# Kernel tuning notes

Measured on AMD Instinct MI355X. Metric: run time of the kernel, lower is better.

## Reference

```python
import jax, jax.numpy as jnp
import numpy as np

EPS = 1e-12  # tf.math.l2_normalize default epsilon

def l2norm(x, axis=-1):
    s = jnp.sum(x * x, axis=axis, keepdims=True)
    return x * jax.lax.rsqrt(jnp.maximum(s, EPS))

def setup_inputs() -> dict:
    key = jax.random.key(0)
    ks = jax.random.split(key, 8)
    B, N, M, D_IN, D_OUT = 8, 4096, 2048, 256, 128
    Y = jax.random.normal(ks[0], (B, N, D_IN), dtype=jnp.float32)
    indices_ = jax.random.randint(ks[1], (B, M), 0, N)
    he = lambda k, fan_in, shape: jax.random.normal(k, shape, jnp.float32) * jnp.sqrt(2.0 / fan_in)
    kernel_query = he(ks[2], D_IN, (D_IN, D_OUT))
    b_query = jnp.zeros((D_OUT,), jnp.float32)
    kernel_key = he(ks[3], D_IN, (D_IN, D_OUT))
    b_key = jnp.zeros((D_OUT,), jnp.float32)
    kernel_value_w = he(ks[4], D_IN, (D_IN, D_OUT))
    kernel_value_b = jnp.zeros((D_OUT,), jnp.float32)
    return {"Y": Y, "indices_": indices_, "kernel_query": kernel_query, "b_query": b_query,
            "kernel_key": kernel_key, "b_key": b_key,
            "kernel_value_w": kernel_value_w, "kernel_value_b": kernel_value_b}

def reference(Y, indices_, kernel_query, b_query, kernel_key, b_key, kernel_value_w, kernel_value_b):
    # Gather same indices for Q/K/V (queries=keys=values=Y in the self block)
    g = jnp.take_along_axis(Y, indices_[..., None], axis=1)      # [B, m, d_in]
    d_in = Y.shape[-1]                                           # scale uses pre-projection dim (as in source)
    Q = jnp.einsum('bmd,de->bme', g, kernel_query) + b_query     # [B, m, d_out]
    K = jnp.einsum('bmd,de->bme', g, kernel_key) + b_key
    V = jax.nn.relu(jnp.einsum('bmd,de->bme', g, kernel_value_w) + kernel_value_b)
    scores = jnp.einsum('bme,bne->bmn', Q, K) / jnp.sqrt(jnp.float32(d_in))  # [B, m, m]
    att = jax.nn.softmax(scores, axis=-1)                        # valid_lens=None path -> plain softmax
    att_emb = l2norm(jnp.einsum('bmn,bne->bme', att, V))         # attention_embedding: l2-normalize, not sum-divide
    out = l2norm(V + att_emb)                                    # residual_connection with l2 normalize
    return (out, att)
```

## Files before the change

### kernel.cpp

```cpp
#include <hip/hip_runtime.h>
#include <hip/hip_bf16.h>
#include <math.h>

typedef __attribute__((ext_vector_type(8))) short short8;
typedef __attribute__((ext_vector_type(16))) float f32x16;

constexpr int B = 8, N = 4096, M = 2048, DIN = 256, DOUT = 128;
constexpr float SCORE_SCALE = 0.0625f;

__device__ __forceinline__ unsigned short f2b(float x) {
    unsigned int u = __builtin_bit_cast(unsigned int, x);
    u += 0x7fffu + ((u >> 16) & 1u);
    return (unsigned short)(u >> 16);
}

__global__ __launch_bounds__(128) void k_proj(
    const float* __restrict__ Y, const int* __restrict__ idx,
    const float* __restrict__ Wq, const float* __restrict__ bq,
    const float* __restrict__ Wk, const float* __restrict__ bk,
    const float* __restrict__ Wv, const float* __restrict__ bv,
    unsigned short* __restrict__ Qb, unsigned short* __restrict__ Kb,
    unsigned short* __restrict__ Vb, float* __restrict__ Vf)
{
    constexpr int TM = 8;
    __shared__ float g[TM][DIN];
    const int rm0 = blockIdx.x * TM;
    const int b = rm0 / M;
    const int t = threadIdx.x;
    #pragma unroll
    for (int r = 0; r < TM; ++r) {
        const int id = idx[rm0 + r];
        const float2* src = (const float2*)(Y + ((size_t)b * N + id) * DIN);
        ((float2*)g[r])[t] = src[t];
    }
    __syncthreads();

    float aq[TM], ak[TM], av[TM];
    #pragma unroll
    for (int r = 0; r < TM; ++r) { aq[r] = 0.f; ak[r] = 0.f; av[r] = 0.f; }

    for (int d = 0; d < DIN; d += 4) {
        float wq[4], wk[4], wv[4];
        #pragma unroll
        for (int u = 0; u < 4; ++u) {
            wq[u] = Wq[(d + u) * DOUT + t];
            wk[u] = Wk[(d + u) * DOUT + t];
            wv[u] = Wv[(d + u) * DOUT + t];
        }
        #pragma unroll
        for (int r = 0; r < TM; ++r) {
            const float4 gv = *(const float4*)&g[r][d];
            aq[r] = fmaf(gv.x, wq[0], fmaf(gv.y, wq[1], fmaf(gv.z, wq[2], fmaf(gv.w, wq[3], aq[r]))));
            ak[r] = fmaf(gv.x, wk[0], fmaf(gv.y, wk[1], fmaf(gv.z, wk[2], fmaf(gv.w, wk[3], ak[r]))));
            av[r] = fmaf(gv.x, wv[0], fmaf(gv.y, wv[1], fmaf(gv.z, wv[2], fmaf(gv.w, wv[3], av[r]))));
        }
    }
    #pragma unroll
    for (int r = 0; r < TM; ++r) {
        const size_t o = (size_t)(rm0 + r) * DOUT + t;
        const float q = aq[r] + bq[t];
        const float k = ak[r] + bk[t];
        const float v = fmaxf(av[r] + bv[t], 0.0f);
        Qb[o] = f2b(q);
        Kb[o] = f2b(k);
        Vb[o] = f2b(v);
        Vf[o] = v;
    }
}

#define SMEM_BYTES 99328

__global__ __launch_bounds__(512) void k_attn(
    const unsigned short* __restrict__ Qb, const unsigned short* __restrict__ Kb,
    const unsigned short* __restrict__ Vb, const float* __restrict__ Vf,
    float* __restrict__ out, float* __restrict__ att)
{
    extern __shared__ char smem[];
    char* Qs = smem;
    char* Ks = smem + 16384;
    char* Ps = smem + 49152;
    char* Vt = smem + 65536;
    float* sums = (float*)(smem + 98304);

    const int t = threadIdx.x;
    const int l = t & 63, wv = t >> 6;
    const int h = l >> 5;
    const int b = blockIdx.y;
    const int m0 = blockIdx.x * 64;
    const size_t bM = (size_t)b * M;

    const int mw = wv >> 2, nw = wv & 3;
    const int amw = wv & 1, aew = wv >> 1;

    int rowf[16];
    #pragma unroll
    for (int r = 0; r < 16; ++r) rowf[r] = (r & 3) + 8 * (r >> 2) + 4 * h;

    {
        const int row = t >> 3, ce = (t & 7) * 16;
        const uint4* src = (const uint4*)(Qb + (bM + m0 + row) * 128 + ce);
        const uint4 q0 = src[0], q1 = src[1];
        *(uint4*)(Qs + row * 256 + ((ce * 2)      ^ ((row & 7) << 4))) = q0;
        *(uint4*)(Qs + row * 256 + ((ce * 2 + 16) ^ ((row & 7) << 4))) = q1;
    }

    const int krow = t >> 2, kce = (t & 3) * 32;
    const int vrow = t & 127, veb = (t >> 7) * 32;
    const int arow = mw * 32 + (l & 31);
    const int brow = nw * 32 + (l & 31);
    const int kb0 = h * 16;

    uint4 kreg[4], vreg[4];
    {
        const uint4* src = (const uint4*)(Kb + (bM + krow) * 128 + kce);
        #pragma unroll
        for (int u = 0; u < 4; ++u) kreg[u] = src[u];
    }

    float sum_part[16];
    #pragma unroll
    for (int r = 0; r < 16; ++r) sum_part[r] = 0.f;

    for (int c = 0; c < 16; ++c) {
        __syncthreads();
        #pragma unroll
        for (int u = 0; u < 4; ++u)
            *(uint4*)(Ks + krow * 256 + ((kce * 2 + u * 16) ^ ((krow & 7) << 4))) = kreg[u];
        __syncthreads();
        if (c < 15) {
            const uint4* src = (const uint4*)(Kb + (bM + (c + 1) * 128 + krow) * 128 + kce);
            #pragma unroll
            for (int u = 0; u < 4; ++u) kreg[u] = src[u];
        }
        f32x16 acc;
        #pragma unroll
        for (int i = 0; i < 16; ++i) acc[i] = 0.f;
        #pragma unroll
        for (int kc = 0; kc < 8; ++kc) {
            const short8 a  = *(const short8*)(Qs + arow * 256 + ((kc * 32 + kb0) ^ ((arow & 7) << 4)));
            const short8 bb = *(const short8*)(Ks + brow * 256 + ((kc * 32 + kb0) ^ ((brow & 7) << 4)));
            acc = __builtin_amdgcn_mfma_f32_32x32x16_bf16(a, bb, acc, 0, 0, 0);
        }
        #pragma unroll
        for (int r = 0; r < 16; ++r)
            sum_part[r] += __expf(acc[r] * SCORE_SCALE);
    }

    #pragma unroll
    for (int r = 0; r < 16; ++r) {
        float s = sum_part[r];
        #pragma unroll
        for (int off = 1; off <= 16; off <<= 1) s += __shfl_xor(s, off, 64);
        sum_part[r] = s;
    }
    if ((l & 31) == 0) {
        #pragma unroll
        for (int r = 0; r < 16; ++r) sums[nw * 64 + mw * 32 + rowf[r]] = sum_part[r];
    }
    __syncthreads();
    float inv_s[16];
    #pragma unroll
    for (int r = 0; r < 16; ++r) {
        const int rw = mw * 32 + rowf[r];
        inv_s[r] = 1.0f / (sums[rw] + sums[64 + rw] + sums[128 + rw] + sums[192 + rw]);
    }

    {
        const uint4* sk = (const uint4*)(Kb + (bM + krow) * 128 + kce);
        #pragma unroll
        for (int u = 0; u < 4; ++u) kreg[u] = sk[u];
        const uint4* sv = (const uint4*)(Vb + (bM + vrow) * 128 + veb);
        #pragma unroll
        for (int u = 0; u < 4; ++u) vreg[u] = sv[u];
    }
    f32x16 accv;
    #pragma unroll
    for (int i = 0; i < 16; ++i) accv[i] = 0.f;

    float* attb = att + bM * M;
    const int parow = amw * 32 + (l & 31);
    const int vbrow = aew * 32 + (l & 31);

    for (int c = 0; c < 16; ++c) {
        __syncthreads();
        #pragma unroll
        for (int u = 0; u < 4; ++u)
            *(uint4*)(Ks + krow * 256 + ((kce * 2 + u * 16) ^ ((krow & 7) << 4))) = kreg[u];
        #pragma unroll
        for (int u = 0; u < 4; ++u) {
            union { uint4 q; unsigned short us[8]; } cv; cv.q = vreg[u];
            #pragma unroll
            for (int j = 0; j < 8; ++j) {
                const int e = veb + u * 8 + j;
                *(unsigned short*)(Vt + e * 256 + ((vrow * 2) ^ ((e & 7) << 4))) = cv.us[j];
            }
        }
        __syncthreads();
        if (c < 15) {
            const uint4* sk = (const uint4*)(Kb + (bM + (c + 1) * 128 + krow) * 128 + kce);
            #pragma unroll
            for (int u = 0; u < 4; ++u) kreg[u] = sk[u];
            const uint4* sv = (const uint4*)(Vb + (bM + (c + 1) * 128 + vrow) * 128 + veb);
            #pragma unroll
            for (int u = 0; u < 4; ++u) vreg[u] = sv[u];
        }
        f32x16 acc;
        #pragma unroll
        for (int i = 0; i < 16; ++i) acc[i] = 0.f;
        #pragma unroll
        for (int kc = 0; kc < 8; ++kc) {
            const short8 a  = *(const short8*)(Qs + arow * 256 + ((kc * 32 + kb0) ^ ((arow & 7) << 4)));
            const short8 bb = *(const short8*)(Ks + brow * 256 + ((kc * 32 + kb0) ^ ((brow & 7) << 4)));
            acc = __builtin_amdgcn_mfma_f32_32x32x16_bf16(a, bb, acc, 0, 0, 0);
        }
        const int ncol = c * 128 + nw * 32 + (l & 31);
        #pragma unroll
        for (int r = 0; r < 16; ++r) {
            const float p = __expf(acc[r] * SCORE_SCALE) * inv_s[r];
            const int prow = mw * 32 + rowf[r];
            attb[(size_t)(m0 + prow) * M + ncol] = p;
            *(unsigned short*)(Ps + prow * 256 + (((nw * 32 + (l & 31)) * 2) ^ ((prow & 7) << 4))) = f2b(p);
        }
        __syncthreads();
        #pragma unroll
        for (int kc = 0; kc < 8; ++kc) {
            const short8 pa = *(const short8*)(Ps + parow * 256 + ((kc * 32 + kb0) ^ ((parow & 7) << 4)));
            const short8 vb = *(const short8*)(Vt + vbrow * 256 + ((kc * 32 + kb0) ^ ((vbrow & 7) << 4)));
            accv = __builtin_amdgcn_mfma_f32_32x32x16_bf16(pa, vb, accv, 0, 0, 0);
        }
    }

    __syncthreads();
    float* Es = (float*)smem;
    #pragma unroll
    for (int r = 0; r < 16; ++r)
        Es[(amw * 32 + rowf[r]) * 129 + aew * 32 + (l & 31)] = accv[r];
    __syncthreads();
    #pragma unroll
    for (int rr = 0; rr < 8; ++rr) {
        const int row = wv * 8 + rr;
        const float e0 = Es[row * 129 + l];
        const float e1 = Es[row * 129 + l + 64];
        float ss = fmaf(e0, e0, e1 * e1);
        #pragma unroll
        for (int off = 32; off >= 1; off >>= 1) ss += __shfl_xor(ss, off, 64);
        const float rs = rsqrtf(fmaxf(ss, 1e-12f));
        const float v0 = Vf[(bM + m0 + row) * 128 + l];
        const float v1 = Vf[(bM + m0 + row) * 128 + l + 64];
        const float t0 = v0 + e0 * rs, t1 = v1 + e1 * rs;
        float s2 = fmaf(t0, t0, t1 * t1);
        #pragma unroll
        for (int off = 32; off >= 1; off >>= 1) s2 += __shfl_xor(s2, off, 64);
        const float rs2 = rsqrtf(fmaxf(s2, 1e-12f));
        const size_t o = (bM + m0 + row) * 128;
        out[o + l] = t0 * rs2;
        out[o + l + 64] = t1 * rs2;
    }
}

extern "C" void kernel_launch(void* const* d_in, const int* in_sizes, int n_in,
                              void* d_out, int out_size, void* d_ws, size_t ws_size,
                              hipStream_t stream)
{
    const float* Y  = (const float*)d_in[0];
    const int*  idx = (const int*)d_in[1];
    const float* Wq = (const float*)d_in[2];
    const float* bq = (const float*)d_in[3];
    const float* Wk = (const float*)d_in[4];
    const float* bk = (const float*)d_in[5];
    const float* Wv = (const float*)d_in[6];
    const float* bv = (const float*)d_in[7];

    float* out = (float*)d_out;
    float* att = out + (size_t)B * M * DOUT;

    unsigned short* Qb = (unsigned short*)d_ws;
    unsigned short* Kb = Qb + (size_t)B * M * DOUT;
    unsigned short* Vb = Kb + (size_t)B * M * DOUT;
    float*          Vf = (float*)(Vb + (size_t)B * M * DOUT);

    hipFuncSetAttribute((const void*)k_attn, hipFuncAttributeMaxDynamicSharedMemorySize, SMEM_BYTES);

    k_proj<<<B * M / 8, 128, 0, stream>>>(Y, idx, Wq, bq, Wk, bk, Wv, bv, Qb, Kb, Vb, Vf);
    k_attn<<<dim3(M / 64, B), 512, SMEM_BYTES, stream>>>(Qb, Kb, Vb, Vf, out, att);
}
```

Before: 325.4 us.

## Load Q/K/V MFMA fragments directly from global and pre-transpose V in projection

Result: faster. 307.1 us (-5.6%).

```diff
diff --git a/kernel.cpp b/kernel.cpp
--- a/kernel.cpp
+++ b/kernel.cpp
@@ -14,136 +14,132 @@
     return (unsigned short)(u >> 16);
 }
 
-__global__ __launch_bounds__(128) void k_proj(
+__global__ __launch_bounds__(512) void k_proj(
     const float* __restrict__ Y, const int* __restrict__ idx,
     const float* __restrict__ Wq, const float* __restrict__ bq,
     const float* __restrict__ Wk, const float* __restrict__ bk,
     const float* __restrict__ Wv, const float* __restrict__ bv,
     unsigned short* __restrict__ Qb, unsigned short* __restrict__ Kb,
-    unsigned short* __restrict__ Vb, float* __restrict__ Vf)
+    unsigned short* __restrict__ Vbt, float* __restrict__ Vf)
 {
-    constexpr int TM = 8;
-    __shared__ float g[TM][DIN];
-    const int rm0 = blockIdx.x * TM;
-    const int b = rm0 / M;
+    __shared__ float g[32][DIN];
+    const int b = blockIdx.x;
+    const int m0 = blockIdx.y * 32;
     const int t = threadIdx.x;
-    #pragma unroll
-    for (int r = 0; r < TM; ++r) {
-        const int id = idx[rm0 + r];
-        const float2* src = (const float2*)(Y + ((size_t)b * N + id) * DIN);
-        ((float2*)g[r])[t] = src[t];
+    const int e = t & 127, q = t >> 7;
+
+    {
+        const int gr = t >> 4, gc = t & 15;
+        const int id = idx[b * M + m0 + gr];
+        const float4* src = (const float4*)(Y + ((size_t)b * N + id) * DIN);
+        float4* dst = (float4*)g[gr];
+        #pragma unroll
+        for (int j = 0; j < 4; ++j) dst[gc + 16 * j] = src[gc + 16 * j];
     }
     __syncthreads();
 
-    float aq[TM], ak[TM], av[TM];
-    #pragma unroll
-    for (int r = 0; r < TM; ++r) { aq[r] = 0.f; ak[r] = 0.f; av[r] = 0.f; }
+    float aq[8], ak[8], av[8];
+    #pragma unroll
+    for (int r = 0; r < 8; ++r) { aq[r] = 0.f; ak[r] = 0.f; av[r] = 0.f; }
 
     for (int d = 0; d < DIN; d += 4) {
         float wq[4], wk[4], wv[4];
         #pragma unroll
         for (int u = 0; u < 4; ++u) {
-            wq[u] = Wq[(d + u) * DOUT + t];
-            wk[u] = Wk[(d + u) * DOUT + t];
-            wv[u] = Wv[(d + u) * DOUT + t];
-        }
-        #pragma unroll
-        for (int r = 0; r < TM; ++r) {
-            const float4 gv = *(const float4*)&g[r][d];
+            wq[u] = Wq[(d + u) * DOUT + e];
+            wk[u] = Wk[(d + u) * DOUT + e];
+            wv[u] = Wv[(d + u) * DOUT + e];
+        }
+        #pragma unroll
+        for (int r = 0; r < 8; ++r) {
+            const float4 gv = *(const float4*)&g[q * 8 + r][d];
             aq[r] = fmaf(gv.x, wq[0], fmaf(gv.y, wq[1], fmaf(gv.z, wq[2], fmaf(gv.w, wq[3], aq[r]))));
             ak[r] = fmaf(gv.x, wk[0], fmaf(gv.y, wk[1], fmaf(gv.z, wk[2], fmaf(gv.w, wk[3], ak[r]))));
             av[r] = fmaf(gv.x, wv[0], fmaf(gv.y, wv[1], fmaf(gv.z, wv[2], fmaf(gv.w, wv[3], av[r]))));
         }
     }
-    #pragma unroll
-    for (int r = 0; r < TM; ++r) {
-        const size_t o = (size_t)(rm0 + r) * DOUT + t;
-        const float q = aq[r] + bq[t];
-        const float k = ak[r] + bk[t];
-        const float v = fmaxf(av[r] + bv[t], 0.0f);
-        Qb[o] = f2b(q);
-        Kb[o] = f2b(k);
-        Vb[o] = f2b(v);
-        Vf[o] = v;
-    }
-}
-
-#define SMEM_BYTES 99328
-
-__global__ __launch_bounds__(512) void k_attn(
+
+    const float bqe = bq[e], bke = bk[e], bve = bv[e];
+    unsigned short vus[8];
+    #pragma unroll
+    for (int r = 0; r < 8; ++r) {
+        const size_t o = ((size_t)b * M + m0 + q * 8 + r) * DOUT + e;
+        const float qv = aq[r] + bqe;
+        const float kv = ak[r] + bke;
+        const float vv = fmaxf(av[r] + bve, 0.0f);
+        Qb[o] = f2b(qv);
+        Kb[o] = f2b(kv);
+        Vf[o] = vv;
+        vus[r] = f2b(vv);
+    }
+    *(uint4*)(Vbt + ((size_t)b * DOUT + e) * M + m0 + q * 8) = *(uint4*)vus;
+}
+
+__global__ __launch_bounds__(256) void k_attn(
     const unsigned short* __restrict__ Qb, const unsigned short* __restrict__ Kb,
-    const unsigned short* __restrict__ Vb, const float* __restrict__ Vf,
+    const unsigned short* __restrict__ Vbt, const float* __restrict__ Vf,
     float* __restrict__ out, float* __restrict__ att)
 {
-    extern __shared__ char smem[];
-    char* Qs = smem;
-    char* Ks = smem + 16384;
-    char* Ps = smem + 49152;
-    char* Vt = smem + 65536;
-    float* sums = (float*)(smem + 98304);
+    __shared__ char Ps[32 * 256];
+    __shared__ float Es[32][132];
+    __shared__ float sums[4][32];
 
     const int t = threadIdx.x;
     const int l = t & 63, wv = t >> 6;
-    const int h = l >> 5;
-    const int b = blockIdx.y;
-    const int m0 = blockIdx.x * 64;
+    const int h = l >> 5, ln = l & 31;
+    const int b = blockIdx.x;
+    const int m0 = blockIdx.y * 32;
     const size_t bM = (size_t)b * M;
-
-    const int mw = wv >> 2, nw = wv & 3;
-    const int amw = wv & 1, aew = wv >> 1;
+    const int nw = wv;
+    const int ew = wv;
 
     int rowf[16];
     #pragma unroll
     for (int r = 0; r < 16; ++r) rowf[r] = (r & 3) + 8 * (r >> 2) + 4 * h;
 
+    short8 qf[8];
     {
-        const int row = t >> 3, ce = (t & 7) * 16;
-        const uint4* src = (const uint4*)(Qb + (bM + m0 + row) * 128 + ce);
-        const uint4 q0 = src[0], q1 = src[1];
-        *(uint4*)(Qs + row * 256 + ((ce * 2)      ^ ((row & 7) << 4))) = q0;
-        *(uint4*)(Qs + row * 256 + ((ce * 2 + 16) ^ ((row & 7) << 4))) = q1;
-    }
-
-    const int krow = t >> 2, kce = (t & 3) * 32;
-    const int vrow = t & 127, veb = (t >> 7) * 32;
-    const int arow = mw * 32 + (l & 31);
-    const int brow = nw * 32 + (l & 31);
-    const int kb0 = h * 16;
-
-    uint4 kreg[4], vreg[4];
-    {
-        const uint4* src = (const uint4*)(Kb + (bM + krow) * 128 + kce);
-        #pragma unroll
-        for (int u = 0; u < 4; ++u) kreg[u] = src[u];
-    }
-
+        const unsigned short* qrow = Qb + (bM + m0 + ln) * DOUT + h * 8;
+        #pragma unroll
+        for (int kc = 0; kc < 8; ++kc) qf[kc] = *(const short8*)(qrow + kc * 16);
+    }
+
+    const unsigned short* Kbase = Kb + (bM + nw * 32 + ln) * DOUT + h * 8;
+    const unsigned short* Vbase = Vbt + ((size_t)b * DOUT + ew * 32 + ln) * M + h * 8;
+
+    short8 kf0[8], kf1[8];
+    #pragma unroll
+    for (int kc = 0; kc < 8; ++kc) kf0[kc] = *(const short8*)(Kbase + kc * 16);
     float sum_part[16];
     #pragma unroll
     for (int r = 0; r < 16; ++r) sum_part[r] = 0.f;
 
-    for (int c = 0; c < 16; ++c) {
-        __syncthreads();
-        #pragma unroll
-        for (int u = 0; u < 4; ++u)
-            *(uint4*)(Ks + krow * 256 + ((kce * 2 + u * 16) ^ ((krow & 7) << 4))) = kreg[u];
-        __syncthreads();
-        if (c < 15) {
-            const uint4* src = (const uint4*)(Kb + (bM + (c + 1) * 128 + krow) * 128 + kce);
+    #pragma unroll 1
+    for (int cp = 0; cp < 8; ++cp) {
+        const int c0 = cp * 2;
+        #pragma unroll
+        for (int kc = 0; kc < 8; ++kc)
+            kf1[kc] = *(const short8*)(Kbase + (size_t)(c0 + 1) * 128 * DOUT + kc * 16);
+        f32x16 acc;
+        #pragma unroll
+        for (int i = 0; i < 16; ++i) acc[i] = 0.f;
+        #pragma unroll
+        for (int kc = 0; kc < 8; ++kc)
+            acc = __builtin_amdgcn_mfma_f32_32x32x16_bf16(qf[kc], kf0[kc], acc, 0, 0, 0);
+        #pragma unroll
+        for (int r = 0; r < 16; ++r) sum_part[r] += __expf(acc[r] * SCORE_SCALE);
+        if (cp < 7) {
             #pragma unroll
-            for (int u = 0; u < 4; ++u) kreg[u] = src[u];
-        }
-        f32x16 acc;
+            for (int kc = 0; kc < 8; ++kc)
+                kf0[kc] = *(const short8*)(Kbase + (size_t)(c0 + 2) * 128 * DOUT + kc * 16);
+        }
         #pragma unroll
         for (int i = 0; i < 16; ++i) acc[i] = 0.f;
         #pragma unroll
-        for (int kc = 0; kc < 8; ++kc) {
-            const short8 a  = *(const short8*)(Qs + arow * 256 + ((kc * 32 + kb0) ^ ((arow & 7) << 4)));
-            const short8 bb = *(const short8*)(Ks + brow * 256 + ((kc * 32 + kb0) ^ ((brow & 7) << 4)));
-            acc = __builtin_amdgcn_mfma_f32_32x32x16_bf16(a, bb, acc, 0, 0, 0);
-        }
-        #pragma unroll
-        for (int r = 0; r < 16; ++r)
-            sum_part[r] += __expf(acc[r] * SCORE_SCALE);
+        for (int kc = 0; kc < 8; ++kc)
+            acc = __builtin_amdgcn_mfma_f32_32x32x16_bf16(qf[kc], kf1[kc], acc, 0, 0, 0);
+        #pragma unroll
+        for (int r = 0; r < 16; ++r) sum_part[r] += __expf(acc[r] * SCORE_SCALE);
     }
 
     #pragma unroll
@@ -153,106 +149,85 @@
         for (int off = 1; off <= 16; off <<= 1) s += __shfl_xor(s, off, 64);
         sum_part[r] = s;
     }
-    if ((l & 31) == 0) {
-        #pragma unroll
-        for (int r = 0; r < 16; ++r) sums[nw * 64 + mw * 32 + rowf[r]] = sum_part[r];
+    if (ln == 0) {
+        #pragma unroll
+        for (int r = 0; r < 16; ++r) sums[nw][rowf[r]] = sum_part[r];
     }
     __syncthreads();
     float inv_s[16];
     #pragma unroll
     for (int r = 0; r < 16; ++r) {
-        const int rw = mw * 32 + rowf[r];
-        inv_s[r] = 1.0f / (sums[rw] + sums[64 + rw] + sums[128 + rw] + sums[192 + rw]);
-    }
-
-    {
-        const uint4* sk = (const uint4*)(Kb + (bM + krow) * 128 + kce);
-        #pragma unroll
-        for (int u = 0; u < 4; ++u) kreg[u] = sk[u];
-        const uint4* sv = (const uint4*)(Vb + (bM + vrow) * 128 + veb);
-        #pragma unroll
-        for (int u = 0; u < 4; ++u) vreg[u] = sv[u];
-    }
+        const int rw = rowf[r];
+        inv_s[r] = 1.0f / (sums[0][rw] + sums[1][rw] + sums[2][rw] + sums[3][rw]);
+    }
+
     f32x16 accv;
     #pragma unroll
     for (int i = 0; i < 16; ++i) accv[i] = 0.f;
-
     float* attb = att + bM * M;
-    const int parow = amw * 32 + (l & 31);
-    const int vbrow = aew * 32 + (l & 31);
-
-    for (int c = 0; c < 16; ++c) {
-        __syncthreads();
-        #pragma unroll
-        for (int u = 0; u < 4; ++u)
-            *(uint4*)(Ks + krow * 256 + ((kce * 2 + u * 16) ^ ((krow & 7) << 4))) = kreg[u];
-        #pragma unroll
-        for (int u = 0; u < 4; ++u) {
-            union { uint4 q; unsigned short us[8]; } cv; cv.q = vreg[u];
+
+    auto pv_phase = [&](short8 (&cur)[8], short8 (&nxt)[8], int c, bool pf) {
+        short8 vf[8];
+        #pragma unroll
+        for (int kc = 0; kc < 8; ++kc)
+            vf[kc] = *(const short8*)(Vbase + (size_t)c * 128 + kc * 16);
+        f32x16 acc;
+        #pragma unroll
+        for (int i = 0; i < 16; ++i) acc[i] = 0.f;
+        #pragma unroll
+        for (int kc = 0; kc < 8; ++kc)
+            acc = __builtin_amdgcn_mfma_f32_32x32x16_bf16(qf[kc], cur[kc], acc, 0, 0, 0);
+        if (pf) {
             #pragma unroll
-            for (int j = 0; j < 8; ++j) {
-                const int e = veb + u * 8 + j;
-                *(unsigned short*)(Vt + e * 256 + ((vrow * 2) ^ ((e & 7) << 4))) = cv.us[j];
-            }
-        }
-        __syncthreads();
-        if (c < 15) {
-            const uint4* sk = (const uint4*)(Kb + (bM + (c + 1) * 128 + krow) * 128 + kce);
-            #pragma unroll
-            for (int u = 0; u < 4; ++u) kreg[u] = sk[u];
-            const uint4* sv = (const uint4*)(Vb + (bM + (c + 1) * 128 + vrow) * 128 + veb);
-            #pragma unroll
-            for (int u = 0; u < 4; ++u) vreg[u] = sv[u];
-        }
-        f32x16 acc;
-        #pragma unroll
-        for (int i = 0; i < 16; ++i) acc[i] = 0.f;
-        #pragma unroll
-        for (int kc = 0; kc < 8; ++kc) {
-            const short8 a  = *(const short8*)(Qs + arow * 256 + ((kc * 32 + kb0) ^ ((arow & 7) << 4)));
-            const short8 bb = *(const short8*)(Ks + brow * 256 + ((kc * 32 + kb0) ^ ((brow & 7) << 4)));
-            acc = __builtin_amdgcn_mfma_f32_32x32x16_bf16(a, bb, acc, 0, 0, 0);
-        }
-        const int ncol = c * 128 + nw * 32 + (l & 31);
+            for (int kc = 0; kc < 8; ++kc)
+                nxt[kc] = *(const short8*)(Kbase + (size_t)(c + 1) * 128 * DOUT + kc * 16);
+        }
+        const int ncol = c * 128 + nw * 32 + ln;
         #pragma unroll
         for (int r = 0; r < 16; ++r) {
             const float p = __expf(acc[r] * SCORE_SCALE) * inv_s[r];
-            const int prow = mw * 32 + rowf[r];
-            attb[(size_t)(m0 + prow) * M + ncol] = p;
-            *(unsigned short*)(Ps + prow * 256 + (((nw * 32 + (l & 31)) * 2) ^ ((prow & 7) << 4))) = f2b(p);
+            const int prow = rowf[r];
+            __builtin_nontemporal_store(p, &attb[(size_t)(m0 + prow) * M + ncol]);
+            *(unsigned short*)(Ps + prow * 256 + (((nw * 32 + ln) * 2) ^ ((prow & 7) << 4))) = f2b(p);
         }
         __syncthreads();
         #pragma unroll
         for (int kc = 0; kc < 8; ++kc) {
-            const short8 pa = *(const short8*)(Ps + parow * 256 + ((kc * 32 + kb0) ^ ((parow & 7) << 4)));
-            const short8 vb = *(const short8*)(Vt + vbrow * 256 + ((kc * 32 + kb0) ^ ((vbrow & 7) << 4)));
-            accv = __builtin_amdgcn_mfma_f32_32x32x16_bf16(pa, vb, accv, 0, 0, 0);
-        }
-    }
-
-    __syncthreads();
-    float* Es = (float*)smem;
+            const short8 pa = *(const short8*)(Ps + ln * 256 + ((kc * 32 + h * 16) ^ ((ln & 7) << 4)));
+            accv = __builtin_amdgcn_mfma_f32_32x32x16_bf16(pa, vf[kc], accv, 0, 0, 0);
+        }
+        __syncthreads();
+    };
+
+    #pragma unroll
+    for (int kc = 0; kc < 8; ++kc) kf0[kc] = *(const short8*)(Kbase + kc * 16);
+    #pragma unroll 1
+    for (int cp = 0; cp < 8; ++cp) {
+        pv_phase(kf0, kf1, cp * 2, true);
+        pv_phase(kf1, kf0, cp * 2 + 1, cp < 7);
+    }
+
     #pragma unroll
     for (int r = 0; r < 16; ++r)
-        Es[(amw * 32 + rowf[r]) * 129 + aew * 32 + (l & 31)] = accv[r];
+        Es[rowf[r]][ew * 32 + ln] = accv[r];
     __syncthreads();
     #pragma unroll
     for (int rr = 0; rr < 8; ++rr) {
         const int row = wv * 8 + rr;
-        const float e0 = Es[row * 129 + l];
-        const float e1 = Es[row * 129 + l + 64];
+        const float e0 = Es[row][l];
+        const float e1 = Es[row][l + 64];
         float ss = fmaf(e0, e0, e1 * e1);
         #pragma unroll
         for (int off = 32; off >= 1; off >>= 1) ss += __shfl_xor(ss, off, 64);
         const float rs = rsqrtf(fmaxf(ss, 1e-12f));
-        const float v0 = Vf[(bM + m0 + row) * 128 + l];
-        const float v1 = Vf[(bM + m0 + row) * 128 + l + 64];
+        const float v0 = Vf[(bM + m0 + row) * DOUT + l];
+        const float v1 = Vf[(bM + m0 + row) * DOUT + l + 64];
         const float t0 = v0 + e0 * rs, t1 = v1 + e1 * rs;
         float s2 = fmaf(t0, t0, t1 * t1);
         #pragma unroll
         for (int off = 32; off >= 1; off >>= 1) s2 += __shfl_xor(s2, off, 64);
         const float rs2 = rsqrtf(fmaxf(s2, 1e-12f));
-        const size_t o = (bM + m0 + row) * 128;
+        const size_t o = (bM + m0 + row) * DOUT;
         out[o + l] = t0 * rs2;
         out[o + l + 64] = t1 * rs2;
     }
@@ -274,13 +249,11 @@
     float* out = (float*)d_out;
     float* att = out + (size_t)B * M * DOUT;
 
-    unsigned short* Qb = (unsigned short*)d_ws;
-    unsigned short* Kb = Qb + (size_t)B * M * DOUT;
-    unsigned short* Vb = Kb + (size_t)B * M * DOUT;
-    float*          Vf = (float*)(Vb + (size_t)B * M * DOUT);
-
-    hipFuncSetAttribute((const void*)k_attn, hipFuncAttributeMaxDynamicSharedMemorySize, SMEM_BYTES);
-
-    k_proj<<<B * M / 8, 128, 0, stream>>>(Y, idx, Wq, bq, Wk, bk, Wv, bv, Qb, Kb, Vb, Vf);
-    k_attn<<<dim3(M / 64, B), 512, SMEM_BYTES, stream>>>(Qb, Kb, Vb, Vf, out, att);
-}
+    unsigned short* Qb  = (unsigned short*)d_ws;
+    unsigned short* Kb  = Qb + (size_t)B * M * DOUT;
+    unsigned short* Vbt = Kb + (size_t)B * M * DOUT;
+    float*          Vf  = (float*)(Vbt + (size_t)B * M * DOUT);
+
+    k_proj<<<dim3(8, M / 32), 512, 0, stream>>>(Y, idx, Wq, bq, Wk, bk, Wv, bv, Qb, Kb, Vbt, Vf);
+    k_attn<<<dim3(8, M / 32), 256, 0, stream>>>(Qb, Kb, Vbt, Vf, out, att);
+}
```
